# Performance work log

Measured on AMD Instinct MI355X. Metric: run time of the kernel, lower is better.

## Reference

```python
import jax, jax.numpy as jnp
import numpy as np

NEG_SLOPE = 0.2

def gat_conv(x, edge_index, W, a_src, a_dst, b):
    # PyG GATConv, heads=1, eval mode (dropout off), add_self_loops=True
    N = x.shape[0]
    h = x @ W                                   # [N, C]
    loops = jnp.arange(N, dtype=edge_index.dtype)
    src = jnp.concatenate([edge_index[0], loops])
    dst = jnp.concatenate([edge_index[1], loops])
    s_src = h @ a_src                            # [N]
    s_dst = h @ a_dst                            # [N]
    e = s_src[src] + s_dst[dst]                  # [E+N]
    e = jnp.where(e > 0, e, NEG_SLOPE * e)       # leaky_relu
    # segment softmax over destination neighborhoods
    m = jax.ops.segment_max(e, dst, num_segments=N)
    ex = jnp.exp(e - m[dst])
    denom = jax.ops.segment_sum(ex, dst, num_segments=N)
    alpha = ex / denom[dst]                      # [E+N]
    out = jax.ops.segment_sum(alpha[:, None] * h[src], dst, num_segments=N)
    return out + b

def setup_inputs() -> dict:
    key = jax.random.key(0)
    ks = jax.random.split(key, 10)
    N, F_in, H, C, E = 100000, 256, 128, 40, 1600000
    x = jax.random.normal(ks[0], (N, F_in), dtype=jnp.float32)
    edge_index = jax.random.randint(ks[1], (2, E), 0, N, dtype=jnp.int64)
    s1 = 1.0 / np.sqrt(F_in)
    s2 = 1.0 / np.sqrt(H)
    W1 = jax.random.normal(ks[2], (F_in, H), dtype=jnp.float32) * s1
    a_src1 = jax.random.normal(ks[3], (H,), dtype=jnp.float32) * s2
    a_dst1 = jax.random.normal(ks[4], (H,), dtype=jnp.float32) * s2
    b1 = jnp.zeros((H,), dtype=jnp.float32)
    W2 = jax.random.normal(ks[5], (H, C), dtype=jnp.float32) * s2
    a_src2 = jax.random.normal(ks[6], (C,), dtype=jnp.float32) * 0.1
    a_dst2 = jax.random.normal(ks[7], (C,), dtype=jnp.float32) * 0.1
    b2 = jnp.zeros((C,), dtype=jnp.float32)
    return {"x": x, "edge_index": edge_index, "W1": W1, "a_src1": a_src1,
            "a_dst1": a_dst1, "b1": b1, "W2": W2, "a_src2": a_src2,
            "a_dst2": a_dst2, "b2": b2}

def reference(x, edge_index, W1, a_src1, a_dst1, b1, W2, a_src2, a_dst2, b2):
    h = gat_conv(x, edge_index, W1, a_src1, a_dst1, b1)
    h = jax.nn.relu(h)
    # dropout(p=0.6) is identity in eval mode
    h = gat_conv(h, edge_index, W2, a_src2, a_dst2, b2)
    return jax.nn.log_softmax(h, axis=1)
```

## Files before the change

### kernel.cpp

```cpp
#include <hip/hip_runtime.h>
#include <math.h>

#define NEG_SLOPE 0.2f
#define CAP 64
#define NB 64
#define NBUCKET 1563
#define PSTRIDE 1564
#define CHUNK 2048
#define NCHK 782

typedef __attribute__((ext_vector_type(8))) short short8;
typedef __attribute__((ext_vector_type(4))) short short4v;
typedef __attribute__((ext_vector_type(4))) float f32x4;
typedef __attribute__((ext_vector_type(2))) float f32x2;

__device__ inline unsigned short f2bf(float f) {
    union { float f; unsigned u; } x; x.f = f;
    unsigned r = x.u + 0x7FFFu + ((x.u >> 16) & 1u);
    return (unsigned short)(r >> 16);
}

__device__ __forceinline__ void gload_lds16(const void* g, void* l) {
    __builtin_amdgcn_global_load_lds(
        (const __attribute__((address_space(1))) void*)g,
        (__attribute__((address_space(3))) void*)l, 16, 0, 0);
}


__global__ __launch_bounds__(256) void front_kernel(
    const int* __restrict__ ei, unsigned* __restrict__ bbuf,
    int* __restrict__ pref, int E,
    const float* __restrict__ W1, const float* __restrict__ W2,
    short* __restrict__ bsw1, short* __restrict__ bsw2)
{
    __shared__ int fsm[PSTRIDE + 2 * CHUNK + 4];
    const int tid = threadIdx.x;

    if (blockIdx.x < NCHK) {
        int* lc = fsm;
        int* ls = fsm + PSTRIDE;
        int* ld = fsm + PSTRIDE + CHUNK;
        int* ws = fsm + PSTRIDE + 2 * CHUNK;
        const int q = blockIdx.x;
        const int base = q * CHUNK;
        int n = E - base; if (n > CHUNK) n = CHUNK;

        for (int b = tid; b < NBUCKET; b += 256) lc[b] = 0;
        __syncthreads();
        for (int i = tid; i < n; i += 256) {
            int s = ei[base + i];
            int d = ei[E + base + i];
            ls[i] = s;
            ld[i] = d;
            atomicAdd(&lc[d >> 6], 1);
        }
        __syncthreads();

        const int base0 = tid * 7;
        int loc[7];
        int run = 0;
        #pragma unroll
        for (int j = 0; j < 7; j++) {
            int idx = base0 + j;
            int v = (idx < NBUCKET) ? lc[idx] : 0;
            loc[j] = run;
            run += v;
        }
        const int lane = tid & 63, w = tid >> 6;
        int inc = run;
        #pragma unroll
        for (int off = 1; off < 64; off <<= 1) {
            int t2 = __shfl_up(inc, off);
            if (lane >= off) inc += t2;
        }
        if (lane == 63) ws[w] = inc;
        __syncthreads();
        int wbase = 0;
        #pragma unroll
        for (int i = 0; i < 4; i++) if (i < w) wbase += ws[i];
        int excl = wbase + inc - run;
        __syncthreads();
        int* pr = pref + (size_t)q * PSTRIDE;
        #pragma unroll
        for (int j = 0; j < 7; j++) {
            int idx = base0 + j;
            if (idx < NBUCKET) {
                int e = excl + loc[j];
                pr[idx] = e;
                lc[idx] = e;
            }
        }
        if (tid == 0) pr[NBUCKET] = n;
        __syncthreads();

        unsigned* bp = bbuf + (size_t)q * CHUNK;
        for (int i = tid; i < n; i += 256) {
            int d = ld[i];
            int pos = atomicAdd(&lc[d >> 6], 1);
            bp[pos] = (unsigned)ls[i] | ((unsigned)(d & 63) << 17);
        }
    } else {
        int t = (blockIdx.x - NCHK) * 256 + tid;
        if (t < 4096) {
            int lane = t & 63;
            int f = t >> 6;
            int k_step = f & 7;
            int n_tile = f >> 3;
            int n  = n_tile * 16 + (lane & 15);
            int k0 = k_step * 32 + (lane >> 4) * 8;
            short8 v;
            #pragma unroll
            for (int j = 0; j < 8; j++)
                v[j] = (short)f2bf(W1[(size_t)(k0 + j) * 128 + n]);
            ((short8*)bsw1)[t] = v;
        } else if (t < 4096 + 768) {
            int u = t - 4096;
            int lane = u & 63;
            int f = u >> 6;
            int k_step = f & 3;
            int n_tile = f >> 2;
            int n  = n_tile * 16 + (lane & 15);
            int k0 = k_step * 32 + (lane >> 4) * 8;
            short8 v;
            #pragma unroll
            for (int j = 0; j < 8; j++)
                v[j] = (n < 40) ? (short)f2bf(W2[(size_t)(k0 + j) * 40 + n]) : (short)0;
            ((short8*)bsw2)[u] = v;
        }
    }
}

__global__ __launch_bounds__(256, 2) void mid_kernel(
    const unsigned* __restrict__ bbuf, const int* __restrict__ pref,
    int* __restrict__ csr, int* __restrict__ sorted, int* __restrict__ clsCnt,
    const float* __restrict__ x, const short* __restrict__ bsw,
    const float* __restrict__ a_src, const float* __restrict__ a_dst,
    unsigned char* __restrict__ h1, float* __restrict__ s_src,
    float* __restrict__ s_dst, int M)
{
    __shared__ __align__(16) char smem[16896];
    const int tid = threadIdx.x;
    const int bi = blockIdx.x;
    const int vb = bi >> 1;

    if ((bi & 1) == 0) {
        int* lcnt = (int*)smem;
        int (*lcsr)[CAP] = (int(*)[CAP])(smem + 256);
        int* chist = (int*)(smem + 256 + 16384);
        int* cbase = (int*)(smem + 256 + 16384 + 16);

        const int b = vb;
        const int nb = b * NB;

        if (tid < NB) lcnt[tid] = 0;
        if (tid < 4) chist[tid] = 0;
        __syncthreads();

        if (tid < NB && nb + tid < M) {
            int pos = atomicAdd(&lcnt[tid], 1);
            if (pos < CAP) lcsr[tid][pos] = nb + tid;
        }

        for (int q = tid; q < NCHK; q += 256) {
            const int* pr = pref + (size_t)q * PSTRIDE + b;
            int p0 = pr[0];
            int p1 = pr[1];
            const unsigned* bp = bbuf + (size_t)q * CHUNK;
            for (int j = p0; j < p1; j++) {
                unsigned v = bp[j];
                int dl = v >> 17;
                int pos = atomicAdd(&lcnt[dl], 1);
                if (pos < CAP) lcsr[dl][pos] = v & 0x1FFFF;
            }
        }
        __syncthreads();

        const int4* __restrict__ srcp = (const int4*)&lcsr[0][0];
        int4* __restrict__ dstp = (int4*)(csr + (size_t)nb * CAP);
        #pragma unroll 4
        for (int j = tid; j < NB * CAP / 4; j += 256) dstp[j] = srcp[j];

        int deg = 0, cls = 0, pos = 0;
        bool isNode = (tid < NB && nb + tid < M);
        if (isNode) {
            deg = lcnt[tid]; if (deg > CAP) deg = CAP;
            cls = (deg - 1) >> 4;
            pos = atomicAdd(&chist[cls], 1);
        }
        __syncthreads();
        if (tid < 4) cbase[tid] = chist[tid] ? atomicAdd(&clsCnt[tid], chist[tid]) : 0;
        __syncthreads();
        if (isNode)
            sorted[(size_t)cls * M + cbase[cls] + pos] = (nb + tid) | (deg << 17);
        return;
    }

    const int wave = tid >> 6, lane = tid & 63;
    short8* lbs = (short8*)smem;
    const int rowBase = vb * 64;
    const int arow = rowBase + wave * 16 + (lane & 15);
    const int acol0 = (lane >> 4) * 8;
    const bool rv = (arow < M);
    const float* __restrict__ xr = x + (size_t)arow * 256 + acol0;
    const char* __restrict__ bsb = (const char*)bsw;

    auto stage = [&](int buf, int nt) {
        const char* s = bsb + nt * 8192 + wave * 2048 + lane * 16;
        char* d = smem + buf * 8192 + wave * 2048 + lane * 16;
        gload_lds16(s, d);
        gload_lds16(s + 1024, d + 1024);
    };

    stage(0, 0);

    float4 px[8], qx[8];
    #pragma unroll
    for (int k = 0; k < 8; k++) {
        px[k] = make_float4(0.f, 0.f, 0.f, 0.f);
        qx[k] = px[k];
        if (rv) {
            px[k] = *(const float4*)(xr + k * 32);
            qx[k] = *(const float4*)(xr + k * 32 + 4);
        }
    }
    short8 a[8];
    #pragma unroll
    for (int k = 0; k < 8; k++) {
        short8 t;
        t[0] = (short)f2bf(px[k].x); t[1] = (short)f2bf(px[k].y);
        t[2] = (short)f2bf(px[k].z); t[3] = (short)f2bf(px[k].w);
        t[4] = (short)f2bf(qx[k].x); t[5] = (short)f2bf(qx[k].y);
        t[6] = (short)f2bf(qx[k].z); t[7] = (short)f2bf(qx[k].w);
        a[k] = t;
    }

    const int R0 = rowBase + wave * 16 + (lane >> 4) * 4;
    const int Cb = lane & 15;

    float asv[8], adv[8];
    #pragma unroll
    for (int nt = 0; nt < 8; nt++) {
        asv[nt] = a_src[nt * 16 + Cb];
        adv[nt] = a_dst[nt * 16 + Cb];
    }

    stage(1, 1);

    float ss[4] = {0.f, 0.f, 0.f, 0.f};
    float sd[4] = {0.f, 0.f, 0.f, 0.f};
    f32x4 prev = {0.f, 0.f, 0.f, 0.f};
    int wpk[4][4];

    #pragma unroll
    for (int nt = 0; nt < 8; nt++) {
        if (nt == 7) asm volatile("s_waitcnt vmcnt(0)" ::: "memory");
        else         asm volatile("s_waitcnt vmcnt(2)" ::: "memory");
        __builtin_amdgcn_s_barrier();

        short8 breg[8];
        #pragma unroll
        for (int k = 0; k < 8; k++) breg[k] = lbs[(nt & 1) * 512 + k * 64 + lane];
        asm volatile("s_waitcnt lgkmcnt(0)" ::: "memory");
        __builtin_amdgcn_sched_barrier(0);
        __builtin_amdgcn_s_barrier();

        if (nt < 6) stage(nt & 1, nt + 2);

        __builtin_amdgcn_s_setprio(1);
        f32x4 acc = {0.f, 0.f, 0.f, 0.f};
        #pragma unroll
        for (int k = 0; k < 8; k++)
            acc = __builtin_amdgcn_mfma_f32_16x16x32_bf16(a[k], breg[k], acc, 0, 0, 0);
        __builtin_amdgcn_s_setprio(0);

        float as_ = asv[nt], ad_ = adv[nt];
        #pragma unroll
        for (int r2 = 0; r2 < 4; r2++) {
            float v = acc[r2];
            ss[r2] = fmaf(v, as_, ss[r2]);
            sd[r2] = fmaf(v, ad_, sd[r2]);
        }
        if (nt & 1) {
            #pragma unroll
            for (int r2 = 0; r2 < 4; r2++)
                wpk[nt >> 1][r2] = __builtin_amdgcn_cvt_pk_fp8_f32(prev[r2], acc[r2], 0, false);
        } else {
            prev = acc;
        }
    }

    #pragma unroll
    for (int r2 = 0; r2 < 4; r2++) {
        int R = R0 + r2;
        if (R < M) {
            #pragma unroll
            for (int t = 0; t < 4; t++)
                *(unsigned short*)(h1 + (size_t)R * 128 + t * 32 + 2 * Cb) =
                    (unsigned short)wpk[t][r2];
        }
    }
    #pragma unroll
    for (int off = 1; off < 16; off <<= 1) {
        #pragma unroll
        for (int r2 = 0; r2 < 4; r2++) {
            ss[r2] += __shfl_xor(ss[r2], off);
            sd[r2] += __shfl_xor(sd[r2], off);
        }
    }
    if ((lane & 15) == 0) {
        #pragma unroll
        for (int r2 = 0; r2 < 4; r2++) {
            int R = R0 + r2;
            if (R < M) { s_src[R] = ss[r2]; s_dst[R] = sd[r2]; }
        }
    }
}

__global__ __launch_bounds__(256, 4) void agg1_kernel(
    const unsigned char* __restrict__ h, const int* __restrict__ csr,
    const int* __restrict__ sorted, const int* __restrict__ clsCnt,
    const float* __restrict__ s_src, const float* __restrict__ s_dst,
    const float* __restrict__ bias,
    const short* __restrict__ bsw2,
    const float* __restrict__ a_src2, const float* __restrict__ a_dst2,
    unsigned char* __restrict__ h2, float* __restrict__ ss2,
    float* __restrict__ sd2, int N)
{
    __shared__ short lrow[16][136];
    __shared__ int   lnode[16];
    const int tid = threadIdx.x;
    const int lane = tid & 63;
    const int c = lane & 15;
    const int base = lane & 48;
    const int grp = tid >> 4;
    const int g = blockIdx.x * 16 + grp;

    int c0 = clsCnt[0], c01 = c0 + clsCnt[1], c012 = c01 + clsCnt[2];
    int cls, local;
    if (g < c0)        { cls = 0; local = g; }
    else if (g < c01)  { cls = 1; local = g - c0; }
    else if (g < c012) { cls = 2; local = g - c01; }
    else               { cls = 3; local = g - c012; }

    int ent = sorted[(size_t)cls * N + local];
    int n = ent & 0x1FFFF;
    int deg = ent >> 17;
    const int* __restrict__ edges = csr + (size_t)n * CAP;
    float sdn = s_dst[n];

    int s0 = 0, s1 = 0, s2 = 0, s3 = 0;
    float e0 = -1e30f, e1 = -1e30f, e2 = -1e30f, e3 = -1e30f;
    if (c < deg)      { s0 = edges[c];      e0 = s_src[s0] + sdn; }
    if (c + 16 < deg) { s1 = edges[c + 16]; e1 = s_src[s1] + sdn; }
    if (c + 32 < deg) { s2 = edges[c + 32]; e2 = s_src[s2] + sdn; }
    if (c + 48 < deg) { s3 = edges[c + 48]; e3 = s_src[s3] + sdn; }
    e0 = e0 > 0.f ? e0 : NEG_SLOPE * e0;
    e1 = e1 > 0.f ? e1 : NEG_SLOPE * e1;
    e2 = e2 > 0.f ? e2 : NEG_SLOPE * e2;
    e3 = e3 > 0.f ? e3 : NEG_SLOPE * e3;
    float m = fmaxf(fmaxf(e0, e1), fmaxf(e2, e3));
    #pragma unroll
    for (int off = 1; off < 16; off <<= 1) m = fmaxf(m, __shfl_xor(m, off));
    float w0 = (c < deg)      ? __expf(e0 - m) : 0.f;
    float w1 = (c + 16 < deg) ? __expf(e1 - m) : 0.f;
    float w2 = (c + 32 < deg) ? __expf(e2 - m) : 0.f;
    float w3 = (c + 48 < deg) ? __expf(e3 - m) : 0.f;
    float denom = (w0 + w1) + (w2 + w3);
    #pragma unroll
    for (int off = 1; off < 16; off <<= 1) denom += __shfl_xor(denom, off);
    float inv = 1.0f / denom;

    const uint2* __restrict__ hp = (const uint2*)h;
    f32x2 acc0 = {0.f, 0.f}, acc1 = {0.f, 0.f}, acc2 = {0.f, 0.f}, acc3 = {0.f, 0.f};

#define AGG1_BLK(K, SK, WK)                                                  \
    if (16 * K < deg) {                                                      \
        uint2 u[16];                                                         \
        _Pragma("unroll")                                                    \
        for (int jj = 0; jj < 16; jj++) {                                    \
            int sv = __shfl(SK, base + jj);                                  \
            u[jj] = hp[(size_t)sv * 16 + c];                                 \
        }                                                                    \
        _Pragma("unroll")                                                    \
        for (int jj = 0; jj < 16; jj++) {                                    \
            float wv = __shfl(WK, base + jj);                                \
            f32x2 p;                                                         \
            p = __builtin_amdgcn_cvt_pk_f32_fp8(u[jj].x, false); acc0 += p * wv; \
            p = __builtin_amdgcn_cvt_pk_f32_fp8(u[jj].x, true);  acc1 += p * wv; \
            p = __builtin_amdgcn_cvt_pk_f32_fp8(u[jj].y, false); acc2 += p * wv; \
            p = __builtin_amdgcn_cvt_pk_f32_fp8(u[jj].y, true);  acc3 += p * wv; \
        }                                                                    \
    }
    AGG1_BLK(0, s0, w0)
    AGG1_BLK(1, s1, w1)
    AGG1_BLK(2, s2, w2)
    AGG1_BLK(3, s3, w3)
#undef AGG1_BLK

    int cA = 32 * (c >> 2) + 4 * (c & 3);
    float4 bA = *(const float4*)&bias[cA];
    float4 bB = *(const float4*)&bias[cA + 16];
    float r0 = fmaxf(fmaf(acc0.x, inv, bA.x), 0.f);
    float r1 = fmaxf(fmaf(acc1.x, inv, bA.y), 0.f);
    float r2 = fmaxf(fmaf(acc2.x, inv, bA.z), 0.f);
    float r3 = fmaxf(fmaf(acc3.x, inv, bA.w), 0.f);
    float q0 = fmaxf(fmaf(acc0.y, inv, bB.x), 0.f);
    float q1 = fmaxf(fmaf(acc1.y, inv, bB.y), 0.f);
    float q2 = fmaxf(fmaf(acc2.y, inv, bB.z), 0.f);
    float q3 = fmaxf(fmaf(acc3.y, inv, bB.w), 0.f);
    short4v oA = { (short)f2bf(r0), (short)f2bf(r1), (short)f2bf(r2), (short)f2bf(r3) };
    short4v oB = { (short)f2bf(q0), (short)f2bf(q1), (short)f2bf(q2), (short)f2bf(q3) };
    *(short4v*)&lrow[grp][cA] = oA;
    *(short4v*)&lrow[grp][cA + 16] = oB;
    if (c == 0) lnode[grp] = n;
    __syncthreads();

    if (tid >= 64) return;

    const short8* __restrict__ bs = (const short8*)bsw2;
    short8 a[4];
    #pragma unroll
    for (int k = 0; k < 4; k++)
        a[k] = *(const short8*)&lrow[lane & 15][(lane >> 4) * 8 + k * 32];

    float accs[3][4];
    float ssv[4] = {0.f, 0.f, 0.f, 0.f};
    float sdv[4] = {0.f, 0.f, 0.f, 0.f};

    #pragma unroll
    for (int nt = 0; nt < 3; nt++) {
        f32x4 acc = {0.f, 0.f, 0.f, 0.f};
        #pragma unroll
        for (int k = 0; k < 4; k++) {
            short8 b = bs[(nt * 4 + k) * 64 + lane];
            acc = __builtin_amdgcn_mfma_f32_16x16x32_bf16(a[k], b, acc, 0, 0, 0);
        }
        int C = nt * 16 + c;
        bool valid = (C < 40);
        float as_ = valid ? a_src2[C] : 0.f;
        float ad_ = valid ? a_dst2[C] : 0.f;
        #pragma unroll
        for (int r = 0; r < 4; r++) {
            float v = acc[r];
            accs[nt][r] = v;
            ssv[r] = fmaf(v, as_, ssv[r]);
            sdv[r] = fmaf(v, ad_, sdv[r]);
        }
    }
    #pragma unroll
    for (int r = 0; r < 4; r++) {
        int node = lnode[(lane >> 4) * 4 + r];
        int wA = __builtin_amdgcn_cvt_pk_fp8_f32(accs[0][r], accs[1][r], 0, false);
        int wB = __builtin_amdgcn_cvt_pk_fp8_f32(accs[2][r], 0.f, 0, false);
        *(unsigned short*)(h2 + (size_t)node * 64 + 2 * c) = (unsigned short)wA;
        *(unsigned short*)(h2 + (size_t)node * 64 + 32 + 2 * c) = (unsigned short)wB;
    }
    #pragma unroll
    for (int off = 1; off < 16; off <<= 1) {
        #pragma unroll
        for (int r = 0; r < 4; r++) {
            ssv[r] += __shfl_xor(ssv[r], off);
            sdv[r] += __shfl_xor(sdv[r], off);
        }
    }
    if (c == 0) {
        #pragma unroll
        for (int r = 0; r < 4; r++) {
            int node = lnode[(lane >> 4) * 4 + r];
            ss2[node] = ssv[r];
            sd2[node] = sdv[r];
        }
    }
}

__global__ __launch_bounds__(256, 4) void agg2_kernel(
    const unsigned char* __restrict__ h, const int* __restrict__ csr,
    const int* __restrict__ sorted, const int* __restrict__ clsCnt,
    const float* __restrict__ s_src, const float* __restrict__ s_dst,
    const float* __restrict__ bias, float* __restrict__ out, int N)
{
    const int lane = threadIdx.x & 63;
    const int c = lane & 15;
    const int base = lane & 48;
    const int g = blockIdx.x * 16 + (threadIdx.x >> 4);

    int c0 = clsCnt[0], c01 = c0 + clsCnt[1], c012 = c01 + clsCnt[2];
    int cls, local;
    if (g < c0)        { cls = 0; local = g; }
    else if (g < c01)  { cls = 1; local = g - c0; }
    else if (g < c012) { cls = 2; local = g - c01; }
    else               { cls = 3; local = g - c012; }

    int ent = sorted[(size_t)cls * N + local];
    int n = ent & 0x1FFFF;
    int deg = ent >> 17;
    const int* __restrict__ edges = csr + (size_t)n * CAP;
    float sdn = s_dst[n];

    int s0 = 0, s1 = 0, s2 = 0, s3 = 0;
    float e0 = -1e30f, e1 = -1e30f, e2 = -1e30f, e3 = -1e30f;
    if (c < deg)      { s0 = edges[c];      e0 = s_src[s0] + sdn; }
    if (c + 16 < deg) { s1 = edges[c + 16]; e1 = s_src[s1] + sdn; }
    if (c + 32 < deg) { s2 = edges[c + 32]; e2 = s_src[s2] + sdn; }
    if (c + 48 < deg) { s3 = edges[c + 48]; e3 = s_src[s3] + sdn; }
    e0 = e0 > 0.f ? e0 : NEG_SLOPE * e0;
    e1 = e1 > 0.f ? e1 : NEG_SLOPE * e1;
    e2 = e2 > 0.f ? e2 : NEG_SLOPE * e2;
    e3 = e3 > 0.f ? e3 : NEG_SLOPE * e3;
    float m = fmaxf(fmaxf(e0, e1), fmaxf(e2, e3));
    #pragma unroll
    for (int off = 1; off < 16; off <<= 1) m = fmaxf(m, __shfl_xor(m, off));
    float w0 = (c < deg)      ? __expf(e0 - m) : 0.f;
    float w1 = (c + 16 < deg) ? __expf(e1 - m) : 0.f;
    float w2 = (c + 32 < deg) ? __expf(e2 - m) : 0.f;
    float w3 = (c + 48 < deg) ? __expf(e3 - m) : 0.f;
    float denom = (w0 + w1) + (w2 + w3);
    #pragma unroll
    for (int off = 1; off < 16; off <<= 1) denom += __shfl_xor(denom, off);
    float inv = 1.0f / denom;

    const unsigned* __restrict__ hp = (const unsigned*)h;
    f32x2 acc0 = {0.f, 0.f}, acc1 = {0.f, 0.f};

#define AGG2_BLK(K, SK, WK)                                                  \
    if (16 * K < deg) {                                                      \
        unsigned u[16];                                                      \
        _Pragma("unroll")                                                    \
        for (int jj = 0; jj < 16; jj++) {                                    \
            int sv = __shfl(SK, base + jj);                                  \
            u[jj] = hp[(size_t)sv * 16 + c];                                 \
        }                                                                    \
        _Pragma("unroll")                                                    \
        for (int jj = 0; jj < 16; jj++) {                                    \
            float wv = __shfl(WK, base + jj);                                \
            f32x2 p;                                                         \
            p = __builtin_amdgcn_cvt_pk_f32_fp8(u[jj], false); acc0 += p * wv; \
            p = __builtin_amdgcn_cvt_pk_f32_fp8(u[jj], true);  acc1 += p * wv; \
        }                                                                    \
    }
    AGG2_BLK(0, s0, w0)
    AGG2_BLK(1, s1, w1)
    AGG2_BLK(2, s2, w2)
    AGG2_BLK(3, s3, w3)
#undef AGG2_BLK

    float v0 = -1e30f, v1 = -1e30f, v2 = -1e30f, v3 = -1e30f;
    bool has01 = (c < 8), has0 = (c < 12);
    if (has01) {
        v0 = fmaf(acc0.x, inv, bias[2*c]);
        v1 = fmaf(acc0.y, inv, bias[2*c + 16]);
        v2 = fmaf(acc1.x, inv, bias[2*c + 1]);
        v3 = fmaf(acc1.y, inv, bias[2*c + 17]);
    } else if (has0) {
        v0 = fmaf(acc0.x, inv, bias[2*c + 16]);
        v2 = fmaf(acc1.x, inv, bias[2*c + 17]);
    }

    float mx = fmaxf(fmaxf(v0, v1), fmaxf(v2, v3));
    #pragma unroll
    for (int off = 1; off < 16; off <<= 1) mx = fmaxf(mx, __shfl_xor(mx, off));
    float sum = 0.f;
    if (has01) sum = __expf(v0 - mx) + __expf(v1 - mx) + __expf(v2 - mx) + __expf(v3 - mx);
    else if (has0) sum = __expf(v0 - mx) + __expf(v2 - mx);
    #pragma unroll
    for (int off = 1; off < 16; off <<= 1) sum += __shfl_xor(sum, off);
    float lg = mx + __logf(sum);

    if (has01) {
        *(float2*)&out[(size_t)n * 40 + 2*c]      = make_float2(v0 - lg, v2 - lg);
        *(float2*)&out[(size_t)n * 40 + 2*c + 16] = make_float2(v1 - lg, v3 - lg);
    } else if (has0) {
        *(float2*)&out[(size_t)n * 40 + 2*c + 16] = make_float2(v0 - lg, v2 - lg);
    }
}

extern "C" void kernel_launch(void* const* d_in, const int* in_sizes, int n_in,
                              void* d_out, int out_size, void* d_ws, size_t ws_size,
                              hipStream_t stream)
{
    const float* x      = (const float*)d_in[0];
    const int*   ei     = (const int*)d_in[1];
    const float* W1     = (const float*)d_in[2];
    const float* a_src1 = (const float*)d_in[3];
    const float* a_dst1 = (const float*)d_in[4];
    const float* b1     = (const float*)d_in[5];
    const float* W2     = (const float*)d_in[6];
    const float* a_src2 = (const float*)d_in[7];
    const float* a_dst2 = (const float*)d_in[8];
    const float* b2     = (const float*)d_in[9];
    float* out = (float*)d_out;

    const int N = 100000;
    const int E = 1600000;

    char* ws = (char*)d_ws;
    size_t off = 0;
    auto alloc = [&](size_t bytes) -> void* {
        void* p = ws + off;
        off += (bytes + 255) & ~(size_t)255;
        return p;
    };
    unsigned char*  h1b  = (unsigned char*)alloc((size_t)N * 128);
    unsigned char*  h2b  = (unsigned char*)alloc((size_t)N * 64);
    int*   csr    = (int*)alloc((size_t)NBUCKET * NB * CAP * 4);
    int*   sorted = (int*)alloc((size_t)4 * N * 4);
    float* ss1  = (float*)alloc((size_t)N * 4);
    float* sd1  = (float*)alloc((size_t)N * 4);
    float* ss2  = (float*)alloc((size_t)N * 4);
    float* sd2  = (float*)alloc((size_t)N * 4);
    short* bsw1 = (short*)alloc((size_t)4096 * 8 * 2);
    short* bsw2 = (short*)alloc((size_t)768 * 8 * 2);
    int*   clsCnt = (int*)alloc((size_t)4 * 4);
    unsigned* bbuf = (unsigned*)alloc((size_t)NCHK * CHUNK * 4);
    int*   pref = (int*)alloc((size_t)NCHK * PSTRIDE * 4);

    hipMemsetAsync(clsCnt, 0, 16, stream);

    front_kernel<<<dim3(NCHK + 19), dim3(256), 0, stream>>>(
        ei, bbuf, pref, E, W1, W2, bsw1, bsw2);

    mid_kernel<<<dim3(2 * NBUCKET), dim3(256), 0, stream>>>(
        bbuf, pref, csr, sorted, clsCnt,
        x, bsw1, a_src1, a_dst1, h1b, ss1, sd1, N);

    agg1_kernel<<<dim3(N / 16), dim3(256), 0, stream>>>(
        h1b, csr, sorted, clsCnt, ss1, sd1, b1,
        bsw2, a_src2, a_dst2, h2b, ss2, sd2, N);

    agg2_kernel<<<dim3(N / 16), dim3(256), 0, stream>>>(
        h2b, csr, sorted, clsCnt, ss2, sd2, b2, out, N);
}
```

Measured before the change: 280.9 us.

## Double GEMM rows per block in mid_kernel and interleave with CSR blocks

The GEMM half of mid_kernel now computes 128 rows per block instead of 64, reusing each staged B tile from LDS for two MFMA chains (A and B row sets). The grid is reorganised so every third block is a GEMM block and the other two build CSR buckets, giving 782 GEMM blocks alongside 1563 bucket blocks. This halves B-tile staging and barrier overhead per row and adds independent MFMA chains for latency hiding. The cost is higher register pressure from the doubled A fragments and accumulators, which may reduce occupancy.

```diff
diff --git a/kernel.cpp b/kernel.cpp
--- a/kernel.cpp
+++ b/kernel.cpp
@@ -8,6 +8,7 @@
 #define PSTRIDE 1564
 #define CHUNK 2048
 #define NCHK 782
+#define NGEMM 782
 
 typedef __attribute__((ext_vector_type(8))) short short8;
 typedef __attribute__((ext_vector_type(4))) short short4v;
@@ -141,15 +142,16 @@
     __shared__ __align__(16) char smem[16896];
     const int tid = threadIdx.x;
     const int bi = blockIdx.x;
-    const int vb = bi >> 1;
-
-    if ((bi & 1) == 0) {
+    const int q3 = bi / 3, r3 = bi - q3 * 3;
+
+    if (r3 < 2) {
+        const int b = 2 * q3 + r3;
+        if (b >= NBUCKET) return;
         int* lcnt = (int*)smem;
         int (*lcsr)[CAP] = (int(*)[CAP])(smem + 256);
         int* chist = (int*)(smem + 256 + 16384);
         int* cbase = (int*)(smem + 256 + 16384 + 16);
 
-        const int b = vb;
         const int nb = b * NB;
 
         if (tid < NB) lcnt[tid] = 0;
@@ -195,13 +197,18 @@
         return;
     }
 
+    const int vb = q3;
+    if (vb >= NGEMM) return;
     const int wave = tid >> 6, lane = tid & 63;
     short8* lbs = (short8*)smem;
-    const int rowBase = vb * 64;
-    const int arow = rowBase + wave * 16 + (lane & 15);
+    const int rowBase = vb * 128;
+    const int arowA = rowBase + wave * 16 + (lane & 15);
+    const int arowB = arowA + 64;
     const int acol0 = (lane >> 4) * 8;
-    const bool rv = (arow < M);
-    const float* __restrict__ xr = x + (size_t)arow * 256 + acol0;
+    const bool rvA = (arowA < M);
+    const bool rvB = (arowB < M);
+    const float* __restrict__ xrA = x + (size_t)arowA * 256 + acol0;
+    const float* __restrict__ xrB = x + (size_t)arowB * 256 + acol0;
     const char* __restrict__ bsb = (const char*)bsw;
 
     auto stage = [&](int buf, int nt) {
@@ -213,28 +220,52 @@
 
     stage(0, 0);
 
-    float4 px[8], qx[8];
-    #pragma unroll
-    for (int k = 0; k < 8; k++) {
-        px[k] = make_float4(0.f, 0.f, 0.f, 0.f);
-        qx[k] = px[k];
-        if (rv) {
-            px[k] = *(const float4*)(xr + k * 32);
-            qx[k] = *(const float4*)(xr + k * 32 + 4);
-        }
-    }
-    short8 a[8];
-    #pragma unroll
-    for (int k = 0; k < 8; k++) {
-        short8 t;
-        t[0] = (short)f2bf(px[k].x); t[1] = (short)f2bf(px[k].y);
-        t[2] = (short)f2bf(px[k].z); t[3] = (short)f2bf(px[k].w);
-        t[4] = (short)f2bf(qx[k].x); t[5] = (short)f2bf(qx[k].y);
-        t[6] = (short)f2bf(qx[k].z); t[7] = (short)f2bf(qx[k].w);
-        a[k] = t;
-    }
-
-    const int R0 = rowBase + wave * 16 + (lane >> 4) * 4;
+    short8 aA[8], aB[8];
+    {
+        float4 px[8], qx[8];
+        #pragma unroll
+        for (int k = 0; k < 8; k++) {
+            px[k] = make_float4(0.f, 0.f, 0.f, 0.f);
+            qx[k] = px[k];
+            if (rvA) {
+                px[k] = *(const float4*)(xrA + k * 32);
+                qx[k] = *(const float4*)(xrA + k * 32 + 4);
+            }
+        }
+        #pragma unroll
+        for (int k = 0; k < 8; k++) {
+            short8 t;
+            t[0] = (short)f2bf(px[k].x); t[1] = (short)f2bf(px[k].y);
+            t[2] = (short)f2bf(px[k].z); t[3] = (short)f2bf(px[k].w);
+            t[4] = (short)f2bf(qx[k].x); t[5] = (short)f2bf(qx[k].y);
+            t[6] = (short)f2bf(qx[k].z); t[7] = (short)f2bf(qx[k].w);
+            aA[k] = t;
+        }
+    }
+    {
+        float4 px[8], qx[8];
+        #pragma unroll
+        for (int k = 0; k < 8; k++) {
+            px[k] = make_float4(0.f, 0.f, 0.f, 0.f);
+            qx[k] = px[k];
+            if (rvB) {
+                px[k] = *(const float4*)(xrB + k * 32);
+                qx[k] = *(const float4*)(xrB + k * 32 + 4);
+            }
+        }
+        #pragma unroll
+        for (int k = 0; k < 8; k++) {
+            short8 t;
+            t[0] = (short)f2bf(px[k].x); t[1] = (short)f2bf(px[k].y);
+            t[2] = (short)f2bf(px[k].z); t[3] = (short)f2bf(px[k].w);
+            t[4] = (short)f2bf(qx[k].x); t[5] = (short)f2bf(qx[k].y);
+            t[6] = (short)f2bf(qx[k].z); t[7] = (short)f2bf(qx[k].w);
+            aB[k] = t;
+        }
+    }
+
+    const int R0A = rowBase + wave * 16 + (lane >> 4) * 4;
+    const int R0B = R0A + 64;
     const int Cb = lane & 15;
 
     float asv[8], adv[8];
@@ -246,10 +277,10 @@
 
     stage(1, 1);
 
-    float ss[4] = {0.f, 0.f, 0.f, 0.f};
-    float sd[4] = {0.f, 0.f, 0.f, 0.f};
-    f32x4 prev = {0.f, 0.f, 0.f, 0.f};
-    int wpk[4][4];
+    float ssA[4] = {0.f, 0.f, 0.f, 0.f}, sdA[4] = {0.f, 0.f, 0.f, 0.f};
+    float ssB[4] = {0.f, 0.f, 0.f, 0.f}, sdB[4] = {0.f, 0.f, 0.f, 0.f};
+    f32x4 prevA = {0.f, 0.f, 0.f, 0.f}, prevB = {0.f, 0.f, 0.f, 0.f};
+    int wpkA[4][4], wpkB[4][4];
 
     #pragma unroll
     for (int nt = 0; nt < 8; nt++) {
@@ -267,51 +298,70 @@
         if (nt < 6) stage(nt & 1, nt + 2);
 
         __builtin_amdgcn_s_setprio(1);
-        f32x4 acc = {0.f, 0.f, 0.f, 0.f};
-        #pragma unroll
-        for (int k = 0; k < 8; k++)
-            acc = __builtin_amdgcn_mfma_f32_16x16x32_bf16(a[k], breg[k], acc, 0, 0, 0);
+        f32x4 accA = {0.f, 0.f, 0.f, 0.f};
+        f32x4 accB = {0.f, 0.f, 0.f, 0.f};
+        #pragma unroll
+        for (int k = 0; k < 8; k++) {
+            accA = __builtin_amdgcn_mfma_f32_16x16x32_bf16(aA[k], breg[k], accA, 0, 0, 0);
+            accB = __builtin_amdgcn_mfma_f32_16x16x32_bf16(aB[k], breg[k], accB, 0, 0, 0);
+        }
         __builtin_amdgcn_s_setprio(0);
 
         float as_ = asv[nt], ad_ = adv[nt];
         #pragma unroll
         for (int r2 = 0; r2 < 4; r2++) {
-            float v = acc[r2];
-            ss[r2] = fmaf(v, as_, ss[r2]);
-            sd[r2] = fmaf(v, ad_, sd[r2]);
+            float vA = accA[r2], vB = accB[r2];
+            ssA[r2] = fmaf(vA, as_, ssA[r2]);
+            sdA[r2] = fmaf(vA, ad_, sdA[r2]);
+            ssB[r2] = fmaf(vB, as_, ssB[r2]);
+            sdB[r2] = fmaf(vB, ad_, sdB[r2]);
         }
         if (nt & 1) {
             #pragma unroll
-            for (int r2 = 0; r2 < 4; r2++)
-                wpk[nt >> 1][r2] = __builtin_amdgcn_cvt_pk_fp8_f32(prev[r2], acc[r2], 0, false);
+            for (int r2 = 0; r2 < 4; r2++) {
+                wpkA[nt >> 1][r2] = __builtin_amdgcn_cvt_pk_fp8_f32(prevA[r2], accA[r2], 0, false);
+                wpkB[nt >> 1][r2] = __builtin_amdgcn_cvt_pk_fp8_f32(prevB[r2], accB[r2], 0, false);
+            }
         } else {
-            prev = acc;
+            prevA = accA;
+            prevB = accB;
         }
     }
 
     #pragma unroll
     for (int r2 = 0; r2 < 4; r2++) {
-        int R = R0 + r2;
-        if (R < M) {
+        int RA = R0A + r2;
+        if (RA < M) {
             #pragma unroll
             for (int t = 0; t < 4; t++)
-                *(unsigned short*)(h1 + (size_t)R * 128 + t * 32 + 2 * Cb) =
-                    (unsigned short)wpk[t][r2];
+                *(unsigned short*)(h1 + (size_t)RA * 128 + t * 32 + 2 * Cb) =
+                    (unsigned short)wpkA[t][r2];
+        }
+        int RB = R0B + r2;
+        if (RB < M) {
+            #pragma unroll
+            for (int t = 0; t < 4; t++)
+                *(unsigned short*)(h1 + (size_t)RB * 128 + t * 32 + 2 * Cb) =
+                    (unsigned short)wpkB[t][r2];
         }
     }
     #pragma unroll
     for (int off = 1; off < 16; off <<= 1) {
         #pragma unroll
         for (int r2 = 0; r2 < 4; r2++) {
-            ss[r2] += __shfl_xor(ss[r2], off);
-            sd[r2] += __shfl_xor(sd[r2], off);
+            ssA[r2] += __shfl_xor(ssA[r2], off);
+            sdA[r2] += __shfl_xor(sdA[r2], off);
+            ssB[r2] += __shfl_xor(ssB[r2], off);
+            sdB[r2] += __shfl_xor(sdB[r2], off);
         }
     }
     if ((lane & 15) == 0) {
         #pragma unroll
         for (int r2 = 0; r2 < 4; r2++) {
-            int R = R0 + r2;
-            if (R < M) { s_src[R] = ss[r2]; s_dst[R] = sd[r2]; }
+            int RA = R0A + r2;
+            if (RA < M) { s_src[RA] = ssA[r2]; s_dst[RA] = sdA[r2]; }
+            int RB = R0B + r2;
+            if (RB < M) { s_src[RB] = ssB[r2]; s_dst[RB] = sdB[r2]; }
         }
     }
 }
@@ -619,7 +669,7 @@
     front_kernel<<<dim3(NCHK + 19), dim3(256), 0, stream>>>(
         ei, bbuf, pref, E, W1, W2, bsw1, bsw2);
 
-    mid_kernel<<<dim3(2 * NBUCKET), dim3(256), 0, stream>>>(
+    mid_kernel<<<dim3(3 * NGEMM), dim3(256), 0, stream>>>(
         bbuf, pref, csr, sorted, clsCnt,
         x, bsw1, a_src1, a_dst1, h1b, ss1, sd1, N);
 
```

Result: slower. 287.6 us (+2.4%).
